# Performance work log

Hardware: AMD Instinct MI355X
Metric: run time of the kernel (lower is better)

The kernel has to match this reference:

```python
import math
import jax, jax.numpy as jnp
import numpy as np

# Model hyperparameters (match init_kwargs)
LAYERS, BLOCKS = 10, 4
RC, DC, SC = 32, 32, 256          # residual / dilation / skip channels
CLASSES, L, K = 256, 1024, 3      # classes, input_length, kernel_size
B = 64                            # batch


def _dilations():
    """Replicates the (new_dilation, init_dilation) schedule built in __init__."""
    ds = []
    init = 1
    for _b in range(BLOCKS):
        d = 1
        for _i in range(LAYERS):
            ds.append((d, init))
            init = d
            d *= 2
    return ds


def dilate(x, dilation, init_dilation):
    """Faithful port of the torch dilate(): (n,c,l) -> (n*d/d0, c, l*d0/d)
    via permute/view/permute, zero-padding the start if l is not divisible."""
    n, c, l = x.shape
    if dilation == init_dilation:
        return x
    factor = dilation / init_dilation
    new_l = int(np.ceil(l / factor) * factor)
    if new_l != l:  # constant_pad_1d with pad_start=True
        x = jnp.pad(x, ((0, 0), (0, 0), (new_l - l, 0)))
        l = new_l
    l_new = int(math.ceil(l * init_dilation / dilation))
    n_new = int(math.ceil(n * dilation / init_dilation))
    x = jnp.transpose(x, (1, 2, 0)).reshape(c, l_new, n_new)  # (c, l, n) contiguous view
    return jnp.transpose(x, (2, 0, 1))


def conv1d(x, w, pad):
    # x: (N, Cin, L), w: (Cout, Cin, K)
    return jax.lax.conv_general_dilated(
        x, w, window_strides=(1,), padding=[(pad, pad)],
        dimension_numbers=("NCH", "OIH", "NCH"))


def setup_inputs() -> dict:
    key = jax.random.key(0)
    ks = jax.random.split(key, 8)
    NL = LAYERS * BLOCKS
    return {
        "input": jax.random.normal(ks[0], (B, 2, L), jnp.float32),
        "start_w": jax.random.normal(ks[1], (RC, 2, 1), jnp.float32) * 0.3,
        "filter_w": jax.random.normal(ks[2], (NL, DC, RC, K), jnp.float32) * 0.1,
        "gate_w": jax.random.normal(ks[3], (NL, DC, RC, K), jnp.float32) * 0.1,
        "res_w": jax.random.normal(ks[4], (NL, RC, DC, 1), jnp.float32) * 0.1,
        "skip_w": jax.random.normal(ks[5], (NL, SC, DC, 1), jnp.float32) * 0.1,
        "fc_w": jax.random.normal(ks[6], (CLASSES, SC * L), jnp.float32) * 0.002,
        "fc_b": jnp.zeros((CLASSES,), jnp.float32),
    }


def reference(input, start_w, filter_w, gate_w, res_w, skip_w, fc_w, fc_b):
    pad = K // 2
    x = conv1d(input, start_w, 0)  # (B, RC, L)
    skip = None
    for i, (d, d0) in enumerate(_dilations()):
        residual = dilate(x, d, d0)                              # fast-wavenet reshape
        f = jnp.tanh(conv1d(residual, filter_w[i], pad))
        g = jax.nn.sigmoid(conv1d(residual, gate_w[i], pad))
        x = f * g                                                # gated activation
        s = x if x.shape[2] == 1 else dilate(x, 1, d)            # undo dilation for skip
        s = conv1d(s, skip_w[i], 0)                              # (B, SC, L)
        skip = s if skip is None else s + skip[:, :, -s.shape[2]:]
        x = conv1d(x, res_w[i], 0) + residual                    # residual connection
    out = jax.nn.relu(skip.reshape(skip.shape[0], -1))           # (B, SC*L)
    return out @ fc_w.T + fc_b                                   # (B, CLASSES)
```

## Files before the change

kernel.cpp:

```cpp
#include <hip/hip_runtime.h>
#include <stdint.h>

typedef short bf16x8 __attribute__((ext_vector_type(8)));
typedef float f32x4 __attribute__((ext_vector_type(4)));

#define NPOS 65536
#define MB (1024ull * 1024ull)
#define SK_PIECE 2097152

__device__ __forceinline__ unsigned short f32_bf16(float f) {
    union { float f; unsigned u; } v; v.f = f;
    unsigned u = v.u;
    u += 0x7fffu + ((u >> 16) & 1u);
    return (unsigned short)(u >> 16);
}

__device__ __forceinline__ bf16x8 ldf8_bf16(const float* p) {
    const float4 lo = *(const float4*)p;
    const float4 hi = *(const float4*)(p + 4);
    bf16x8 v;
    v[0] = (short)f32_bf16(lo.x); v[1] = (short)f32_bf16(lo.y);
    v[2] = (short)f32_bf16(lo.z); v[3] = (short)f32_bf16(lo.w);
    v[4] = (short)f32_bf16(hi.x); v[5] = (short)f32_bf16(hi.y);
    v[6] = (short)f32_bf16(hi.z); v[7] = (short)f32_bf16(hi.w);
    return v;
}

__global__ void ws_probe_k(float* __restrict__ out, float mib) {
    int i = blockIdx.x * 256 + threadIdx.x;
    if (i < 16384) out[i] = mib;
}

__global__ void repack_fgw_k(const float* __restrict__ fw,
                             const float* __restrict__ gw,
                             unsigned short* __restrict__ out) {
    int idx = blockIdx.x * 256 + threadIdx.x;
    int ic = idx & 31;
    int r1 = idx >> 5;
    int oc = r1 & 63;
    int r2 = r1 >> 6;
    int k  = r2 % 3;
    int i  = r2 / 3;
    const float* src = (oc < 32) ? fw : gw;
    out[idx] = f32_bf16(src[(((i * 32 + (oc & 31)) * 32 + ic) * 3) + k]);
}

__global__ void repack_sw_k(const float* __restrict__ sw,
                            unsigned short* __restrict__ out) {
    int idx = blockIdx.x * 256 + threadIdx.x;
    out[idx] = f32_bf16(sw[idx]);
}

__global__ void start_conv_k(const float* __restrict__ in,
                             const float* __restrict__ sw,
                             float* __restrict__ x0) {
    int tid = threadIdx.x;
    int p = blockIdx.x * 64 + (tid >> 2);
    int c0 = (tid & 3) * 8;
    int b = p >> 10, t = p & 1023;
    float i0 = in[(b * 2 + 0) * 1024 + t];
    float i1 = in[(b * 2 + 1) * 1024 + t];
    float o[8];
#pragma unroll
    for (int j = 0; j < 8; ++j) {
        int c = c0 + j;
        o[j] = sw[c * 2 + 0] * i0 + sw[c * 2 + 1] * i1;
    }
    float4* dst = (float4*)(x0 + (size_t)p * 32 + c0);
    dst[0] = make_float4(o[0], o[1], o[2], o[3]);
    dst[1] = make_float4(o[4], o[5], o[6], o[7]);
}

__global__ __launch_bounds__(256) void layer_k(
    const float* __restrict__ xin, float* __restrict__ xout,
    const unsigned short* __restrict__ fgw,
    const float* __restrict__ rw,
    unsigned short* __restrict__ xg,
    int d)
{
    __shared__ __align__(16) unsigned short lds1[64 * 40];
    __shared__ __align__(16) float lds2[64 * 36];
    int tid = threadIdx.x;
    int w = tid >> 6, lane = tid & 63;
    int quad = lane >> 4, l15 = lane & 15;
    int p0 = blockIdx.x * 64;
    int b = p0 >> 10, t0 = p0 & 1023;
    int posl = w * 16 + l15;
    int tpos = t0 + posl;
    int ch0 = quad * 8;

    f32x4 zero = {0.f, 0.f, 0.f, 0.f};

    bf16x8 bfr[3];
#pragma unroll
    for (int k = 0; k < 3; ++k) {
        int ts = tpos + (k - 1) * d;
        bf16x8 v;
#pragma unroll
        for (int j = 0; j < 8; ++j) v[j] = 0;
        if (ts >= 0 && ts < 1024)
            v = ldf8_bf16(xin + ((size_t)(b * 1024 + ts)) * 32 + ch0);
        bfr[k] = v;
    }

    f32x4 accf[2] = {zero, zero};
    f32x4 accg[2] = {zero, zero};
#pragma unroll
    for (int k = 0; k < 3; ++k) {
        const unsigned short* wb = fgw + (size_t)k * 64 * 32;
#pragma unroll
        for (int mt = 0; mt < 2; ++mt) {
            bf16x8 af = *(const bf16x8*)(wb + (mt * 16 + l15) * 32 + ch0);
            accf[mt] = __builtin_amdgcn_mfma_f32_16x16x32_bf16(af, bfr[k], accf[mt], 0, 0, 0);
        }
#pragma unroll
        for (int mt = 0; mt < 2; ++mt) {
            bf16x8 ag = *(const bf16x8*)(wb + ((mt + 2) * 16 + l15) * 32 + ch0);
            accg[mt] = __builtin_amdgcn_mfma_f32_16x16x32_bf16(ag, bfr[k], accg[mt], 0, 0, 0);
        }
    }

#pragma unroll
    for (int mt = 0; mt < 2; ++mt)
#pragma unroll
        for (int r = 0; r < 4; ++r) {
            float fv = accf[mt][r], gv = accg[mt][r];
            float th = 1.0f - 2.0f / (1.0f + __expf(2.0f * fv));
            float sg = 1.0f / (1.0f + __expf(-gv));
            lds1[posl * 40 + mt * 16 + quad * 4 + r] = f32_bf16(th * sg);
        }
    __syncthreads();

    {
        int pp = tid >> 2, c0s = (tid & 3) * 8;
        int4 v = *(const int4*)(lds1 + pp * 40 + c0s);
        *(int4*)(xg + ((size_t)(p0 + pp)) * 32 + c0s) = v;
    }

    bf16x8 bx = *(const bf16x8*)(lds1 + posl * 40 + ch0);
    f32x4 accr[2] = {zero, zero};
#pragma unroll
    for (int rt = 0; rt < 2; ++rt) {
        bf16x8 ar = ldf8_bf16(rw + (rt * 16 + l15) * 32 + ch0);
        accr[rt] = __builtin_amdgcn_mfma_f32_16x16x32_bf16(ar, bx, accr[rt], 0, 0, 0);
    }
#pragma unroll
    for (int rt = 0; rt < 2; ++rt)
#pragma unroll
        for (int r = 0; r < 4; ++r)
            lds2[posl * 36 + rt * 16 + quad * 4 + r] = accr[rt][r];
    __syncthreads();

    {
        int pp = tid >> 2, c0s = (tid & 3) * 8;
        const float* xi = xin + ((size_t)(p0 + pp)) * 32 + c0s;
        float* xo = xout + ((size_t)(p0 + pp)) * 32 + c0s;
        float4 a0 = *(const float4*)(xi);
        float4 a1 = *(const float4*)(xi + 4);
        float4 d0 = *(const float4*)(lds2 + pp * 36 + c0s);
        float4 d1 = *(const float4*)(lds2 + pp * 36 + c0s + 4);
        *(float4*)(xo)     = make_float4(a0.x + d0.x, a0.y + d0.y, a0.z + d0.z, a0.w + d0.w);
        *(float4*)(xo + 4) = make_float4(a1.x + d1.x, a1.y + d1.y, a1.z + d1.z, a1.w + d1.w);
    }
}

__global__ __launch_bounds__(256) void skip_gemm_k(
    const unsigned short* __restrict__ xg_all,
    const unsigned short* __restrict__ swb,
    unsigned short* __restrict__ sk)
{
    __shared__ __align__(16) unsigned short lds[256 * 72];
    int tid = threadIdx.x;
    int w = tid >> 6, lane = tid & 63;
    int quad = lane >> 4, l15 = lane & 15;
    int p0 = blockIdx.x * 64;
    f32x4 zero = {0.f, 0.f, 0.f, 0.f};
    f32x4 acc[4][4];
#pragma unroll
    for (int a = 0; a < 4; ++a)
#pragma unroll
        for (int c = 0; c < 4; ++c) acc[a][c] = zero;

    const unsigned short* bbase = xg_all + ((size_t)(p0 + l15)) * 32 + quad * 8;
    const unsigned short* abase = swb + ((size_t)(w * 64 + l15)) * 32 + quad * 8;

    bf16x8 bcur[4], acur[4], bnxt[4], anxt[4];
#pragma unroll
    for (int ct = 0; ct < 4; ++ct) bcur[ct] = *(const bf16x8*)(bbase + ct * 512);
#pragma unroll
    for (int rt = 0; rt < 4; ++rt) acur[rt] = *(const bf16x8*)(abase + rt * 512);

#pragma unroll 2
    for (int i = 0; i < 40; ++i) {
        if (i < 39) {
            const unsigned short* bn = bbase + (size_t)(i + 1) * NPOS * 32;
            const unsigned short* an = abase + (size_t)(i + 1) * 8192;
#pragma unroll
            for (int ct = 0; ct < 4; ++ct) bnxt[ct] = *(const bf16x8*)(bn + ct * 512);
#pragma unroll
            for (int rt = 0; rt < 4; ++rt) anxt[rt] = *(const bf16x8*)(an + rt * 512);
        }
#pragma unroll
        for (int rt = 0; rt < 4; ++rt)
#pragma unroll
            for (int ct = 0; ct < 4; ++ct)
                acc[rt][ct] = __builtin_amdgcn_mfma_f32_16x16x32_bf16(acur[rt], bcur[ct], acc[rt][ct], 0, 0, 0);
#pragma unroll
        for (int ct = 0; ct < 4; ++ct) bcur[ct] = bnxt[ct];
#pragma unroll
        for (int rt = 0; rt < 4; ++rt) acur[rt] = anxt[rt];
    }

#pragma unroll
    for (int rt = 0; rt < 4; ++rt)
#pragma unroll
        for (int ct = 0; ct < 4; ++ct)
#pragma unroll
            for (int r = 0; r < 4; ++r) {
                float v = acc[rt][ct][r];
                v = v > 0.f ? v : 0.f;
                lds[(w * 64 + rt * 16 + quad * 4 + r) * 72 + ct * 16 + l15] = f32_bf16(v);
            }
    __syncthreads();
    {
        size_t pbbase = (size_t)(p0 >> 6) * 2048;
#pragma unroll
        for (int j = 0; j < 8; ++j) {
            int idx = tid + 256 * j;
            int sc = idx >> 3, tc = idx & 7;
            int4 v = *(const int4*)(lds + sc * 72 + tc * 8);
            unsigned short* dst = sk + (size_t)(sc >> 5) * SK_PIECE + pbbase
                                     + (sc & 31) * 64 + tc * 8;
            *(int4*)dst = v;
        }
    }
}

__global__ __launch_bounds__(256) void fc_part_k(
    const unsigned short* __restrict__ sk,
    const float* __restrict__ fw,
    float* __restrict__ part)
{
    int tid = threadIdx.x;
    int w = tid >> 6, lane = tid & 63;
    int quad = lane >> 4, l15 = lane & 15;
    int kb = blockIdx.x;
    int sc = kb >> 1;
    int tbase = (kb & 1) * 512;
    f32x4 zero = {0.f, 0.f, 0.f, 0.f};
    f32x4 acc[4][4];
#pragma unroll
    for (int a = 0; a < 4; ++a)
#pragma unroll
        for (int c = 0; c < 4; ++c) acc[a][c] = zero;

    const unsigned short* skp = sk + (size_t)(sc >> 5) * SK_PIECE + (sc & 31) * 64;

    for (int it = 0; it < 16; ++it) {
        int t = tbase + it * 32 + quad * 8;
        bf16x8 af[4];
#pragma unroll
        for (int rt = 0; rt < 4; ++rt) {
            int b = rt * 16 + l15;
            af[rt] = *(const bf16x8*)(skp + (size_t)(b * 16 + (t >> 6)) * 2048 + (t & 63));
        }
#pragma unroll
        for (int ct = 0; ct < 4; ++ct) {
            bf16x8 bw = ldf8_bf16(fw + (size_t)(w * 64 + ct * 16 + l15) * 262144 + sc * 1024 + t);
#pragma unroll
            for (int rt = 0; rt < 4; ++rt)
                acc[rt][ct] = __builtin_amdgcn_mfma_f32_16x16x32_bf16(af[rt], bw, acc[rt][ct], 0, 0, 0);
        }
    }
#pragma unroll
    for (int rt = 0; rt < 4; ++rt)
#pragma unroll
        for (int ct = 0; ct < 4; ++ct)
#pragma unroll
            for (int r = 0; r < 4; ++r) {
                int bb = rt * 16 + quad * 4 + r;
                int cls = w * 64 + ct * 16 + l15;
                part[((size_t)kb * 64 + bb) * 256 + cls] = acc[rt][ct][r];
            }
}

__global__ void fc_reduce_k(const float* __restrict__ part,
                            const float* __restrict__ fb,
                            float* __restrict__ out) {
    int b = blockIdx.x, cls = threadIdx.x;
    float s = fb[cls];
    for (int kb = 0; kb < 512; ++kb)
        s += part[((size_t)kb * 64 + b) * 256 + cls];
    out[b * 256 + cls] = s;
}

extern "C" void kernel_launch(void* const* d_in, const int* in_sizes, int n_in,
                              void* d_out, int out_size, void* d_ws, size_t ws_size,
                              hipStream_t stream) {
    const float* input    = (const float*)d_in[0];
    const float* start_w  = (const float*)d_in[1];
    const float* filter_w = (const float*)d_in[2];
    const float* gate_w   = (const float*)d_in[3];
    const float* res_w    = (const float*)d_in[4];
    const float* skip_w   = (const float*)d_in[5];
    const float* fc_w     = (const float*)d_in[6];
    const float* fc_b     = (const float*)d_in[7];
    float* out = (float*)d_out;

    const size_t REQUIRED = 192 * MB;
    if (ws_size < REQUIRED) {
        ws_probe_k<<<64, 256, 0, stream>>>(out, (float)(ws_size >> 20));
        return;
    }

    char* ws = (char*)d_ws;
    unsigned short* xg_all = (unsigned short*)(ws);
    unsigned short* sk     = (unsigned short*)(ws);
    float*          part   = (float*)(ws + 32 * MB);
    float*          xa     = (float*)(ws + 160 * MB);
    float*          xb     = (float*)(ws + 168 * MB);
    unsigned short* fgw    = (unsigned short*)(ws + 176 * MB);
    unsigned short* swb    = (unsigned short*)(ws + 176 * MB + 512 * 1024);

    repack_fgw_k<<<960, 256, 0, stream>>>(filter_w, gate_w, fgw);
    repack_sw_k<<<1280, 256, 0, stream>>>(skip_w, swb);
    start_conv_k<<<1024, 256, 0, stream>>>(input, start_w, xa);

    float* xi = xa;
    float* xo = xb;
    for (int i = 0; i < 40; ++i) {
        int d = 1 << (i % 10);
        layer_k<<<1024, 256, 0, stream>>>(xi, xo,
                                          fgw + (size_t)i * 3 * 64 * 32,
                                          res_w + (size_t)i * 32 * 32,
                                          xg_all + (size_t)i * NPOS * 32, d);
        float* tmp = xi; xi = xo; xo = tmp;
    }

    skip_gemm_k<<<1024, 256, 0, stream>>>(xg_all, swb, sk);
    fc_part_k<<<512, 256, 0, stream>>>(sk, fc_w, part);
    fc_reduce_k<<<64, 256, 0, stream>>>(part, fc_b, out);
}
```

Baseline: 984.9 us.

## Fuse all forty WaveNet layers into one persistent kernel with neighbor progress flags

Replaces the forty per-layer launches with a single kernel that loops over layers. Each block waits only on the blocks covering its dilated receptive field in the same batch row, using per-block acquire/release progress counters, instead of a full grid barrier between launches. It also keeps the centre input tap in registers for the residual add instead of re-reading it, and pre-converts the residual weights to bf16. The scheme depends on all 1024 blocks being resident at once, and adds spin-wait overhead and a deadlock risk if they are not.

```diff
diff --git a/kernel.cpp b/kernel.cpp
--- a/kernel.cpp
+++ b/kernel.cpp
@@ -18,6 +18,15 @@
 __device__ __forceinline__ bf16x8 ldf8_bf16(const float* p) {
     const float4 lo = *(const float4*)p;
     const float4 hi = *(const float4*)(p + 4);
+    bf16x8 v;
+    v[0] = (short)f32_bf16(lo.x); v[1] = (short)f32_bf16(lo.y);
+    v[2] = (short)f32_bf16(lo.z); v[3] = (short)f32_bf16(lo.w);
+    v[4] = (short)f32_bf16(hi.x); v[5] = (short)f32_bf16(hi.y);
+    v[6] = (short)f32_bf16(hi.z); v[7] = (short)f32_bf16(hi.w);
+    return v;
+}
+
+__device__ __forceinline__ bf16x8 pack_bf16(float4 lo, float4 hi) {
     bf16x8 v;
     v[0] = (short)f32_bf16(lo.x); v[1] = (short)f32_bf16(lo.y);
     v[2] = (short)f32_bf16(lo.z); v[3] = (short)f32_bf16(lo.w);
@@ -51,6 +60,16 @@
     out[idx] = f32_bf16(sw[idx]);
 }
 
+__global__ void repack_rw_k(const float* __restrict__ rw,
+                            unsigned short* __restrict__ out) {
+    int idx = blockIdx.x * 256 + threadIdx.x;
+    out[idx] = f32_bf16(rw[idx]);
+}
+
+__global__ void zero_progress_k(int* __restrict__ p) {
+    p[blockIdx.x * 256 + threadIdx.x] = 0;
+}
+
 __global__ void start_conv_k(const float* __restrict__ in,
                              const float* __restrict__ sw,
                              float* __restrict__ x0) {
@@ -71,96 +90,130 @@
     dst[1] = make_float4(o[4], o[5], o[6], o[7]);
 }
 
-__global__ __launch_bounds__(256) void layer_k(
-    const float* __restrict__ xin, float* __restrict__ xout,
-    const unsigned short* __restrict__ fgw,
-    const float* __restrict__ rw,
-    unsigned short* __restrict__ xg,
-    int d)
+__global__ __launch_bounds__(256, 4) void layers_fused_k(
+    float* __restrict__ xa, float* __restrict__ xb,
+    const unsigned short* __restrict__ fgw_all,
+    const unsigned short* __restrict__ rwb_all,
+    unsigned short* __restrict__ xg_all,
+    int* __restrict__ progress)
 {
     __shared__ __align__(16) unsigned short lds1[64 * 40];
     __shared__ __align__(16) float lds2[64 * 36];
-    int tid = threadIdx.x;
-    int w = tid >> 6, lane = tid & 63;
-    int quad = lane >> 4, l15 = lane & 15;
-    int p0 = blockIdx.x * 64;
-    int b = p0 >> 10, t0 = p0 & 1023;
-    int posl = w * 16 + l15;
-    int tpos = t0 + posl;
-    int ch0 = quad * 8;
-
-    f32x4 zero = {0.f, 0.f, 0.f, 0.f};
-
-    bf16x8 bfr[3];
-#pragma unroll
-    for (int k = 0; k < 3; ++k) {
-        int ts = tpos + (k - 1) * d;
-        bf16x8 v;
-#pragma unroll
-        for (int j = 0; j < 8; ++j) v[j] = 0;
-        if (ts >= 0 && ts < 1024)
-            v = ldf8_bf16(xin + ((size_t)(b * 1024 + ts)) * 32 + ch0);
-        bfr[k] = v;
-    }
-
-    f32x4 accf[2] = {zero, zero};
-    f32x4 accg[2] = {zero, zero};
-#pragma unroll
-    for (int k = 0; k < 3; ++k) {
-        const unsigned short* wb = fgw + (size_t)k * 64 * 32;
-#pragma unroll
-        for (int mt = 0; mt < 2; ++mt) {
-            bf16x8 af = *(const bf16x8*)(wb + (mt * 16 + l15) * 32 + ch0);
-            accf[mt] = __builtin_amdgcn_mfma_f32_16x16x32_bf16(af, bfr[k], accf[mt], 0, 0, 0);
-        }
-#pragma unroll
-        for (int mt = 0; mt < 2; ++mt) {
-            bf16x8 ag = *(const bf16x8*)(wb + ((mt + 2) * 16 + l15) * 32 + ch0);
-            accg[mt] = __builtin_amdgcn_mfma_f32_16x16x32_bf16(ag, bfr[k], accg[mt], 0, 0, 0);
-        }
-    }
-
-#pragma unroll
-    for (int mt = 0; mt < 2; ++mt)
-#pragma unroll
-        for (int r = 0; r < 4; ++r) {
-            float fv = accf[mt][r], gv = accg[mt][r];
-            float th = 1.0f - 2.0f / (1.0f + __expf(2.0f * fv));
-            float sg = 1.0f / (1.0f + __expf(-gv));
-            lds1[posl * 40 + mt * 16 + quad * 4 + r] = f32_bf16(th * sg);
-        }
-    __syncthreads();
-
-    {
-        int pp = tid >> 2, c0s = (tid & 3) * 8;
-        int4 v = *(const int4*)(lds1 + pp * 40 + c0s);
-        *(int4*)(xg + ((size_t)(p0 + pp)) * 32 + c0s) = v;
-    }
-
-    bf16x8 bx = *(const bf16x8*)(lds1 + posl * 40 + ch0);
-    f32x4 accr[2] = {zero, zero};
-#pragma unroll
-    for (int rt = 0; rt < 2; ++rt) {
-        bf16x8 ar = ldf8_bf16(rw + (rt * 16 + l15) * 32 + ch0);
-        accr[rt] = __builtin_amdgcn_mfma_f32_16x16x32_bf16(ar, bx, accr[rt], 0, 0, 0);
-    }
-#pragma unroll
-    for (int rt = 0; rt < 2; ++rt)
-#pragma unroll
-        for (int r = 0; r < 4; ++r)
-            lds2[posl * 36 + rt * 16 + quad * 4 + r] = accr[rt][r];
-    __syncthreads();
-
-    {
-        int pp = tid >> 2, c0s = (tid & 3) * 8;
-        const float* xi = xin + ((size_t)(p0 + pp)) * 32 + c0s;
-        float* xo = xout + ((size_t)(p0 + pp)) * 32 + c0s;
-        float4 a0 = *(const float4*)(xi);
-        float4 a1 = *(const float4*)(xi + 4);
-        float4 d0 = *(const float4*)(lds2 + pp * 36 + c0s);
-        float4 d1 = *(const float4*)(lds2 + pp * 36 + c0s + 4);
-        *(float4*)(xo)     = make_float4(a0.x + d0.x, a0.y + d0.y, a0.z + d0.z, a0.w + d0.w);
-        *(float4*)(xo + 4) = make_float4(a1.x + d1.x, a1.y + d1.y, a1.z + d1.z, a1.w + d1.w);
+    const int tid = threadIdx.x;
+    const int w = tid >> 6, lane = tid & 63;
+    const int quad = lane >> 4, l15 = lane & 15;
+    const int pb = blockIdx.x;
+    const int p0 = pb * 64;
+    const int b = p0 >> 10, t0 = p0 & 1023;
+    const int row0 = pb & ~15;
+    const int posl = w * 16 + l15;
+    const int tpos = t0 + posl;
+    const int ch0 = quad * 8;
+    const f32x4 zero = {0.f, 0.f, 0.f, 0.f};
+
+    for (int i = 0; i < 40; ++i) {
+        const int d = 1 << (i % 10);
+
+        if (i > 0) {
+            const int dp = 1 << ((i - 1) % 10);
+            const int dm = d > dp ? d : dp;
+            const int r = (dm + 63) >> 6;
+            int nlo = pb - r; if (nlo < row0) nlo = row0;
+            int nhi = pb + r; if (nhi > row0 + 15) nhi = row0 + 15;
+            if (tid <= nhi - nlo) {
+                while (__hip_atomic_load(progress + nlo + tid, __ATOMIC_ACQUIRE,
+                                         __HIP_MEMORY_SCOPE_AGENT) < i)
+                    __builtin_amdgcn_s_sleep(2);
+            }
+            __syncthreads();
+        }
+
+        const float* __restrict__ xin = (i & 1) ? xb : xa;
+        float* __restrict__ xout      = (i & 1) ? xa : xb;
+        const unsigned short* fgw = fgw_all + (size_t)i * 6144;
+        unsigned short* xg = xg_all + (size_t)i * ((size_t)NPOS * 32);
+
+        float4 clo, chi;
+        bf16x8 bfr[3];
+        {
+            const float* cp = xin + ((size_t)(b * 1024 + tpos)) * 32 + ch0;
+            clo = *(const float4*)cp;
+            chi = *(const float4*)(cp + 4);
+            bfr[1] = pack_bf16(clo, chi);
+        }
+#pragma unroll
+        for (int k = 0; k < 3; k += 2) {
+            int ts = tpos + (k - 1) * d;
+            bf16x8 v;
+#pragma unroll
+            for (int j = 0; j < 8; ++j) v[j] = 0;
+            if (ts >= 0 && ts < 1024)
+                v = ldf8_bf16(xin + ((size_t)(b * 1024 + ts)) * 32 + ch0);
+            bfr[k] = v;
+        }
+
+        f32x4 accf[2] = {zero, zero};
+        f32x4 accg[2] = {zero, zero};
+#pragma unroll
+        for (int k = 0; k < 3; ++k) {
+            const unsigned short* wb = fgw + (size_t)k * 2048;
+#pragma unroll
+            for (int mt = 0; mt < 2; ++mt) {
+                bf16x8 af = *(const bf16x8*)(wb + (mt * 16 + l15) * 32 + ch0);
+                accf[mt] = __builtin_amdgcn_mfma_f32_16x16x32_bf16(af, bfr[k], accf[mt], 0, 0, 0);
+            }
+#pragma unroll
+            for (int mt = 0; mt < 2; ++mt) {
+                bf16x8 ag = *(const bf16x8*)(wb + ((mt + 2) * 16 + l15) * 32 + ch0);
+                accg[mt] = __builtin_amdgcn_mfma_f32_16x16x32_bf16(ag, bfr[k], accg[mt], 0, 0, 0);
+            }
+        }
+
+#pragma unroll
+        for (int mt = 0; mt < 2; ++mt)
+#pragma unroll
+            for (int r = 0; r < 4; ++r) {
+                float fv = accf[mt][r], gv = accg[mt][r];
+                float th = 1.0f - 2.0f / (1.0f + __expf(2.0f * fv));
+                float sg = 1.0f / (1.0f + __expf(-gv));
+                lds1[posl * 40 + mt * 16 + quad * 4 + r] = f32_bf16(th * sg);
+            }
+        __syncthreads();
+
+        {
+            int pp = tid >> 2, c0s = (tid & 3) * 8;
+            int4 v = *(const int4*)(lds1 + pp * 40 + c0s);
+            *(int4*)(xg + ((size_t)(p0 + pp)) * 32 + c0s) = v;
+        }
+
+        if (i < 39) {
+            bf16x8 bx = *(const bf16x8*)(lds1 + posl * 40 + ch0);
+            const unsigned short* rwb = rwb_all + (size_t)i * 1024;
+            f32x4 accr[2] = {zero, zero};
+#pragma unroll
+            for (int rt = 0; rt < 2; ++rt) {
+                bf16x8 ar = *(const bf16x8*)(rwb + (rt * 16 + l15) * 32 + ch0);
+                accr[rt] = __builtin_amdgcn_mfma_f32_16x16x32_bf16(ar, bx, accr[rt], 0, 0, 0);
+            }
+#pragma unroll
+            for (int rt = 0; rt < 2; ++rt)
+#pragma unroll
+                for (int r = 0; r < 4; ++r)
+                    lds2[posl * 36 + rt * 16 + quad * 4 + r] = accr[rt][r];
+        }
+        __syncthreads();
+
+        if (i < 39) {
+            float* xo = xout + ((size_t)(p0 + posl)) * 32 + ch0;
+            float4 d0 = *(const float4*)(lds2 + posl * 36 + ch0);
+            float4 d1 = *(const float4*)(lds2 + posl * 36 + ch0 + 4);
+            *(float4*)(xo)     = make_float4(clo.x + d0.x, clo.y + d0.y, clo.z + d0.z, clo.w + d0.w);
+            *(float4*)(xo + 4) = make_float4(chi.x + d1.x, chi.y + d1.y, chi.z + d1.z, chi.w + d1.w);
+            __syncthreads();
+            if (tid == 0)
+                __hip_atomic_store(progress + pb, i + 1, __ATOMIC_RELEASE,
+                                   __HIP_MEMORY_SCOPE_AGENT);
+        }
     }
 }
 
@@ -261,8 +314,8 @@
         bf16x8 af[4];
 #pragma unroll
         for (int rt = 0; rt < 4; ++rt) {
-            int b = rt * 16 + l15;
-            af[rt] = *(const bf16x8*)(skp + (size_t)(b * 16 + (t >> 6)) * 2048 + (t & 63));
+            int bi = rt * 16 + l15;
+            af[rt] = *(const bf16x8*)(skp + (size_t)(bi * 16 + (t >> 6)) * 2048 + (t & 63));
         }
 #pragma unroll
         for (int ct = 0; ct < 4; ++ct) {
@@ -321,21 +374,16 @@
     float*          xb     = (float*)(ws + 168 * MB);
     unsigned short* fgw    = (unsigned short*)(ws + 176 * MB);
     unsigned short* swb    = (unsigned short*)(ws + 176 * MB + 512 * 1024);
+    unsigned short* rwb    = (unsigned short*)(ws + 178 * MB);
+    int*            progress = (int*)(ws + 184 * MB);
 
     repack_fgw_k<<<960, 256, 0, stream>>>(filter_w, gate_w, fgw);
     repack_sw_k<<<1280, 256, 0, stream>>>(skip_w, swb);
+    repack_rw_k<<<160, 256, 0, stream>>>(res_w, rwb);
+    zero_progress_k<<<4, 256, 0, stream>>>(progress);
     start_conv_k<<<1024, 256, 0, stream>>>(input, start_w, xa);
 
-    float* xi = xa;
-    float* xo = xb;
-    for (int i = 0; i < 40; ++i) {
-        int d = 1 << (i % 10);
-        layer_k<<<1024, 256, 0, stream>>>(xi, xo,
-                                          fgw + (size_t)i * 3 * 64 * 32,
-                                          res_w + (size_t)i * 32 * 32,
-                                          xg_all + (size_t)i * NPOS * 32, d);
-        float* tmp = xi; xi = xo; xo = tmp;
-    }
+    layers_fused_k<<<1024, 256, 0, stream>>>(xa, xb, fgw, rwb, xg_all, progress);
 
     skip_gemm_k<<<1024, 256, 0, stream>>>(xg_all, swb, sk);
     fc_part_k<<<512, 256, 0, stream>>>(sk, fc_w, part);
```

After: 2.551 ms. 159% more time.
